# Optimization experiments

Hardware: AMD Instinct MI355X
Metric: run time of the kernel (lower is better)

## Reference

```python
import jax, jax.numpy as jnp
import numpy as np

EPS = 1e-5
G = 8    # groups
K = 3    # kernel_size


def bn(x, gamma, beta, mean, var):
    # inference-mode BatchNorm2d; x: (b,C,H,W), params: (C,)
    inv = gamma / jnp.sqrt(var + EPS)
    return x * inv[None, :, None, None] + (beta - mean * inv)[None, :, None, None]


def gconv1x1(x, w):
    # grouped 1x1 conv; x: (b, g*ci, H, W), w: (g, co, ci) -> (b, g*co, H, W)
    b, C, H, W = x.shape
    g, co, ci = w.shape
    xg = x.reshape(b, g, ci, H, W)
    y = jnp.einsum('bgihw,goi->bgohw', xg, w)
    return y.reshape(b, g * co, H, W)


def unfold3(x):
    # torch.nn.Unfold(k=3, stride=1, dilation=1, padding=1), reshaped to (b, C, 9, H, W)
    b, C, H, W = x.shape
    xp = jnp.pad(x, ((0, 0), (0, 0), (1, 1), (1, 1)))
    patches = [xp[:, :, i:i + H, j:j + W] for i in range(K) for j in range(K)]
    return jnp.stack(patches, axis=2)


def setup_inputs() -> dict:
    key = jax.random.key(0)
    ks = jax.random.split(key, 16)
    f = jax.random.normal
    u = jax.random.uniform
    return {
        'x':  f(ks[0], (2, 256, 128, 128), jnp.float32),
        'w1': f(ks[1], (8, 8, 32), jnp.float32) * 0.1,
        'b1': f(ks[2], (64,), jnp.float32) * 0.1,
        'g1': u(ks[3], (64,), jnp.float32, 0.5, 1.5),
        'be1': f(ks[4], (64,), jnp.float32) * 0.1,
        'm1': f(ks[5], (64,), jnp.float32) * 0.1,
        'v1': u(ks[6], (64,), jnp.float32, 0.5, 1.5),
        'w2': f(ks[7], (8, 10, 8), jnp.float32) * 0.1,
        'b2': f(ks[8], (80,), jnp.float32) * 0.1,
        'g2': u(ks[9], (80,), jnp.float32, 0.5, 1.5),
        'be2': f(ks[10], (80,), jnp.float32) * 0.1,
        'm2': f(ks[11], (80,), jnp.float32) * 0.1,
        'v2': u(ks[12], (80,), jnp.float32, 0.5, 1.5),
        'wv': f(ks[13], (8, 32, 32), jnp.float32) * 0.1,
    }


def reference(x, w1, b1, g1, be1, m1, v1, w2, b2, g2, be2, m2, v2, wv):
    b, C, H, W = x.shape
    # mask_conv: grouped 1x1 conv -> BN -> tanh -> grouped 1x1 conv -> BN
    t = jnp.tanh(bn(gconv1x1(x, w1) + b1[None, :, None, None], g1, be1, m1, v1))
    mn = bn(gconv1x1(t, w2) + b2[None, :, None, None], g2, be2, m2, v2)  # (b, G*(1+K*K), H, W)
    neighbor = mn[:, :G]          # (b, G, H, W)
    mask = mn[:, G:]              # (b, G*K*K, H, W)
    nb = unfold3(neighbor)        # (b, G, 9, H, W)
    logits = mask.reshape(b, G, K * K, H, W) + nb
    attn = jax.nn.softmax(logits, axis=2)               # (b, G, 9, H, W)
    # value path: grouped 1x1 conv (no bias) then unfold
    v = gconv1x1(x, wv)                                  # (b, C, H, W)
    vu = unfold3(v).reshape(b, G, C // G, K * K, H, W)   # (b, G, C/G, 9, H, W)
    out = jnp.einsum('bgkhw,bgckhw->bgchw', attn, vu)    # weighted sum over window
    return out.reshape(b, C, H, W)
```

## Files before the change

kernel.cpp:

```cpp
#include <hip/hip_runtime.h>

#define HW  16384
#define WD  128

#define TS   16
#define HS   18
#define HP   (HS * HS)
#define PRS  20
#define PLS  360

__device__ __forceinline__ unsigned short f2bf(float f) {
    unsigned int u = __builtin_bit_cast(unsigned int, f);
    u += 0x7FFFu + ((u >> 16) & 1u);
    return (unsigned short)(u >> 16);
}
__device__ __forceinline__ float bf2f(unsigned int s) {
    return __builtin_bit_cast(float, (s & 0xFFFFu) << 16);
}
__device__ __forceinline__ float ftanh(float v) {
    const float e = __expf(2.0f * v);
    return 1.0f - __fdividef(2.0f, e + 1.0f);
}

__global__ __launch_bounds__(256) void la_t(
    const float* __restrict__ x,
    const float* __restrict__ w1, const float* __restrict__ b1,
    const float* __restrict__ g1, const float* __restrict__ be1,
    const float* __restrict__ m1, const float* __restrict__ v1,
    ushort4* __restrict__ t4)
{
    const int pix = blockIdx.x * blockDim.x + threadIdx.x;
    const int b   = blockIdx.y;
    const int z   = blockIdx.z;
    const int p   = z >> 1;
    const int h   = z & 1;

    const float* xp = x + (size_t)(b * 256 + p * 32) * HW + pix;
    float xv[32];
#pragma unroll
    for (int c = 0; c < 32; ++c) xv[c] = xp[(size_t)c * HW];

    const float* w1g = w1 + p * 256 + h * 4 * 32;
    float tv[4];
#pragma unroll
    for (int o = 0; o < 4; ++o) {
        float a = 0.f;
#pragma unroll
        for (int ci = 0; ci < 32; ++ci) a = fmaf(xv[ci], w1g[o * 32 + ci], a);
        const int ch = p * 8 + h * 4 + o;
        const float inv = g1[ch] * rsqrtf(v1[ch] + 1e-5f);
        const float add = be1[ch] + (b1[ch] - m1[ch]) * inv;
        tv[o] = ftanh(fmaf(a, inv, add));
    }

    t4[((size_t)((b * 8 + p) * 2 + h)) * HW + pix] =
        make_ushort4(f2bf(tv[0]), f2bf(tv[1]), f2bf(tv[2]), f2bf(tv[3]));
}

__global__ __launch_bounds__(256, 4) void la_fused(
    const float* __restrict__ x,
    const float* __restrict__ w2, const float* __restrict__ b2,
    const float* __restrict__ g2, const float* __restrict__ be2,
    const float* __restrict__ m2, const float* __restrict__ v2,
    const float* __restrict__ wv,
    const ushort4* __restrict__ t4,
    float* __restrict__ out)
{
    __shared__ ushort4 xt[8 * PLS];
    __shared__ float   nbs[PLS];

    const int tid  = threadIdx.x;
    const int bg   = blockIdx.x;
    const int tile = blockIdx.y;
    const int b    = bg >> 3, g = bg & 7;
    const int ty0  = (tile >> 3) * TS;
    const int tx0  = (tile & 7) * TS;

    const float*   xg  = x  + (size_t)(b * 256 + g * 32) * HW;
    const ushort4* t0  = t4 + (size_t)(b * 16) * HW;

    const float inv2n = g2[g] * rsqrtf(v2[g] + 1e-5f);
    const float add2n = be2[g] + (b2[g] - m2[g]) * inv2n;

    for (int hp = tid; hp < HP; hp += 256) {
        const int hy = hp / HS, hx = hp - hy * HS;
        const int iy = ty0 + hy - 1, ix = tx0 + hx - 1;
        const int slot = hy * PRS + hx;
        if (((unsigned)iy < 128u) && ((unsigned)ix < 128u)) {
            const int po = iy * WD + ix;
            float xv[32];
#pragma unroll
            for (int c = 0; c < 32; ++c) xv[c] = xg[(size_t)c * HW + po];
            const ushort4 ta = t0[po];
            const ushort4 tb = t0[(size_t)HW + po];
            float an = 0.f;
            an = fmaf(bf2f(ta.x), w2[g * 8 + 0], an);
            an = fmaf(bf2f(ta.y), w2[g * 8 + 1], an);
            an = fmaf(bf2f(ta.z), w2[g * 8 + 2], an);
            an = fmaf(bf2f(ta.w), w2[g * 8 + 3], an);
            an = fmaf(bf2f(tb.x), w2[g * 8 + 4], an);
            an = fmaf(bf2f(tb.y), w2[g * 8 + 5], an);
            an = fmaf(bf2f(tb.z), w2[g * 8 + 6], an);
            an = fmaf(bf2f(tb.w), w2[g * 8 + 7], an);
            nbs[slot] = fmaf(an, inv2n, add2n);
#pragma unroll
            for (int c4 = 0; c4 < 8; ++c4)
                xt[c4 * PLS + slot] = make_ushort4(
                    f2bf(xv[c4 * 4 + 0]), f2bf(xv[c4 * 4 + 1]),
                    f2bf(xv[c4 * 4 + 2]), f2bf(xv[c4 * 4 + 3]));
        } else {
            const ushort4 z = make_ushort4(0, 0, 0, 0);
#pragma unroll
            for (int c4 = 0; c4 < 8; ++c4) xt[c4 * PLS + slot] = z;
            nbs[slot] = 0.f;
        }
    }
    __syncthreads();

    const int cy  = tid >> 4, cx = tid & 15;
    const int iy  = ty0 + cy, ix = tx0 + cx;
    const int pix = iy * WD + ix;

    const int mc0    = 8 + 9 * g;
    const int pa     = mc0 / 10;
    const int pb     = (mc0 + 8) / 10;
    const int ksplit = 10 - (mc0 - pa * 10);

    float tA[8], tB[8];
    {
        const ushort4 lo = t4[((size_t)((b * 8 + pa) * 2 + 0)) * HW + pix];
        const ushort4 hi = t4[((size_t)((b * 8 + pa) * 2 + 1)) * HW + pix];
        tA[0] = bf2f(lo.x); tA[1] = bf2f(lo.y);
        tA[2] = bf2f(lo.z); tA[3] = bf2f(lo.w);
        tA[4] = bf2f(hi.x); tA[5] = bf2f(hi.y);
        tA[6] = bf2f(hi.z); tA[7] = bf2f(hi.w);
    }
    if (pb != pa) {
        const ushort4 lo = t4[((size_t)((b * 8 + pb) * 2 + 0)) * HW + pix];
        const ushort4 hi = t4[((size_t)((b * 8 + pb) * 2 + 1)) * HW + pix];
        tB[0] = bf2f(lo.x); tB[1] = bf2f(lo.y);
        tB[2] = bf2f(lo.z); tB[3] = bf2f(lo.w);
        tB[4] = bf2f(hi.x); tB[5] = bf2f(hi.y);
        tB[6] = bf2f(hi.z); tB[7] = bf2f(hi.w);
    } else {
#pragma unroll
        for (int o = 0; o < 8; ++o) tB[o] = tA[o];
    }

    float lg[9];
    float mx = -1e30f;
#pragma unroll
    for (int k = 0; k < 9; ++k) {
        const int mc = mc0 + k;
        const int p  = (k < ksplit) ? pa : pb;
        const int o  = mc - p * 10;
        const float* w2p = w2 + p * 80 + o * 8;
        float a = 0.f;
#pragma unroll
        for (int i = 0; i < 8; ++i) {
            const float ti = (k < ksplit) ? tA[i] : tB[i];
            a = fmaf(ti, w2p[i], a);
        }
        const float inv = g2[mc] * rsqrtf(v2[mc] + 1e-5f);
        const float add = be2[mc] + (b2[mc] - m2[mc]) * inv;
        lg[k] = fmaf(a, inv, add) + nbs[(cy + k / 3) * PRS + (cx + k % 3)];
        mx = fmaxf(mx, lg[k]);
    }
    float ssum = 0.f;
#pragma unroll
    for (int k = 0; k < 9; ++k) { lg[k] = __expf(lg[k] - mx); ssum += lg[k]; }
    const float rs = 1.f / ssum;

    float s[32];
#pragma unroll
    for (int c = 0; c < 32; ++c) s[c] = 0.f;
#pragma unroll
    for (int k = 0; k < 9; ++k) {
        const int slot = (cy + k / 3) * PRS + (cx + k % 3);
        const float e = lg[k];
#pragma unroll
        for (int c4 = 0; c4 < 8; ++c4) {
            const ushort4 xv4 = xt[c4 * PLS + slot];
            s[c4 * 4 + 0] = fmaf(e, bf2f(xv4.x), s[c4 * 4 + 0]);
            s[c4 * 4 + 1] = fmaf(e, bf2f(xv4.y), s[c4 * 4 + 1]);
            s[c4 * 4 + 2] = fmaf(e, bf2f(xv4.z), s[c4 * 4 + 2]);
            s[c4 * 4 + 3] = fmaf(e, bf2f(xv4.w), s[c4 * 4 + 3]);
        }
    }

    const float* wvg = wv + g * 1024;
    float* og = out + (size_t)(b * 256 + g * 32) * HW + pix;
#pragma unroll 4
    for (int o = 0; o < 32; ++o) {
        const float* wp = wvg + o * 32;
        float a = 0.f;
#pragma unroll
        for (int ci = 0; ci < 32; ++ci) a = fmaf(s[ci], wp[ci], a);
        __builtin_nontemporal_store(a * rs, og + (size_t)o * HW);
    }
}

extern "C" void kernel_launch(void* const* d_in, const int* in_sizes, int n_in,
                              void* d_out, int out_size, void* d_ws, size_t ws_size,
                              hipStream_t stream)
{
    const float* x   = (const float*)d_in[0];
    const float* w1  = (const float*)d_in[1];
    const float* b1  = (const float*)d_in[2];
    const float* g1  = (const float*)d_in[3];
    const float* be1 = (const float*)d_in[4];
    const float* m1  = (const float*)d_in[5];
    const float* v1  = (const float*)d_in[6];
    const float* w2  = (const float*)d_in[7];
    const float* b2  = (const float*)d_in[8];
    const float* g2  = (const float*)d_in[9];
    const float* be2 = (const float*)d_in[10];
    const float* m2  = (const float*)d_in[11];
    const float* v2  = (const float*)d_in[12];
    const float* wv  = (const float*)d_in[13];

    float* out = (float*)d_out;
    ushort4* t4 = (ushort4*)d_ws;

    dim3 blk(256);
    dim3 gt(HW / 256, 2, 16);
    dim3 grd(16, 64);

    hipLaunchKernelGGL(la_t, gt, blk, 0, stream,
                       x, w1, b1, g1, be1, m1, v1, t4);
    hipLaunchKernelGGL(la_fused, grd, blk, 0, stream,
                       x, w2, b2, g2, be2, m2, v2, wv, t4, out);
}
```

Measured before the change: 126.8 us.

## Precompute bf16 copy of x in first kernel and split output channels across blocks

The first kernel now also writes a bf16 copy of x to workspace, so the fused kernel reads compact bf16 halo data instead of fp32 x. The fused kernel's grid is doubled, with each block computing only 16 of the 32 output channels of the value projection. This cuts the fused kernel's read traffic and per-block register work, and raises parallelism. The cost is an extra bf16 write and read of x, duplicated halo/softmax work across the two half-blocks, and dropping the occupancy hint from the launch bounds.

```diff
diff --git a/kernel.cpp b/kernel.cpp
--- a/kernel.cpp
+++ b/kernel.cpp
@@ -27,7 +27,7 @@
     const float* __restrict__ w1, const float* __restrict__ b1,
     const float* __restrict__ g1, const float* __restrict__ be1,
     const float* __restrict__ m1, const float* __restrict__ v1,
-    ushort4* __restrict__ t4)
+    ushort4* __restrict__ t4, ushort4* __restrict__ xbf)
 {
     const int pix = blockIdx.x * blockDim.x + threadIdx.x;
     const int b   = blockIdx.y;
@@ -40,6 +40,14 @@
 #pragma unroll
     for (int c = 0; c < 32; ++c) xv[c] = xp[(size_t)c * HW];
 
+#pragma unroll
+    for (int j = 0; j < 4; ++j) {
+        const int c4 = h * 4 + j;
+        xbf[((size_t)((b * 8 + p) * 8 + c4)) * HW + pix] = make_ushort4(
+            f2bf(xv[c4 * 4 + 0]), f2bf(xv[c4 * 4 + 1]),
+            f2bf(xv[c4 * 4 + 2]), f2bf(xv[c4 * 4 + 3]));
+    }
+
     const float* w1g = w1 + p * 256 + h * 4 * 32;
     float tv[4];
 #pragma unroll
@@ -57,27 +65,27 @@
         make_ushort4(f2bf(tv[0]), f2bf(tv[1]), f2bf(tv[2]), f2bf(tv[3]));
 }
 
-__global__ __launch_bounds__(256, 4) void la_fused(
-    const float* __restrict__ x,
+__global__ __launch_bounds__(256) void la_fused(
     const float* __restrict__ w2, const float* __restrict__ b2,
     const float* __restrict__ g2, const float* __restrict__ be2,
     const float* __restrict__ m2, const float* __restrict__ v2,
     const float* __restrict__ wv,
-    const ushort4* __restrict__ t4,
+    const ushort4* __restrict__ t4, const ushort4* __restrict__ xbf,
     float* __restrict__ out)
 {
     __shared__ ushort4 xt[8 * PLS];
     __shared__ float   nbs[PLS];
 
     const int tid  = threadIdx.x;
-    const int bg   = blockIdx.x;
+    const int y    = blockIdx.x;
     const int tile = blockIdx.y;
+    const int bg   = y >> 1, h = y & 1;
     const int b    = bg >> 3, g = bg & 7;
     const int ty0  = (tile >> 3) * TS;
     const int tx0  = (tile & 7) * TS;
 
-    const float*   xg  = x  + (size_t)(b * 256 + g * 32) * HW;
-    const ushort4* t0  = t4 + (size_t)(b * 16) * HW;
+    const ushort4* xg = xbf + (size_t)((b * 8 + g) * 8) * HW;
+    const ushort4* t0 = t4  + (size_t)(b * 16) * HW;
 
     const float inv2n = g2[g] * rsqrtf(v2[g] + 1e-5f);
     const float add2n = be2[g] + (b2[g] - m2[g]) * inv2n;
@@ -88,9 +96,6 @@
         const int slot = hy * PRS + hx;
         if (((unsigned)iy < 128u) && ((unsigned)ix < 128u)) {
             const int po = iy * WD + ix;
-            float xv[32];
-#pragma unroll
-            for (int c = 0; c < 32; ++c) xv[c] = xg[(size_t)c * HW + po];
             const ushort4 ta = t0[po];
             const ushort4 tb = t0[(size_t)HW + po];
             float an = 0.f;
@@ -105,9 +110,7 @@
             nbs[slot] = fmaf(an, inv2n, add2n);
 #pragma unroll
             for (int c4 = 0; c4 < 8; ++c4)
-                xt[c4 * PLS + slot] = make_ushort4(
-                    f2bf(xv[c4 * 4 + 0]), f2bf(xv[c4 * 4 + 1]),
-                    f2bf(xv[c4 * 4 + 2]), f2bf(xv[c4 * 4 + 3]));
+                xt[c4 * PLS + slot] = xg[(size_t)c4 * HW + po];
         } else {
             const ushort4 z = make_ushort4(0, 0, 0, 0);
 #pragma unroll
@@ -188,10 +191,10 @@
         }
     }
 
-    const float* wvg = wv + g * 1024;
-    float* og = out + (size_t)(b * 256 + g * 32) * HW + pix;
+    const float* wvg = wv + g * 1024 + h * 16 * 32;
+    float* og = out + (size_t)(b * 256 + g * 32 + h * 16) * HW + pix;
 #pragma unroll 4
-    for (int o = 0; o < 32; ++o) {
+    for (int o = 0; o < 16; ++o) {
         const float* wp = wvg + o * 32;
         float a = 0.f;
 #pragma unroll
@@ -220,14 +223,15 @@
     const float* wv  = (const float*)d_in[13];
 
     float* out = (float*)d_out;
-    ushort4* t4 = (ushort4*)d_ws;
+    ushort4* t4  = (ushort4*)d_ws;
+    ushort4* xbf = t4 + (size_t)32 * HW;
 
     dim3 blk(256);
     dim3 gt(HW / 256, 2, 16);
-    dim3 grd(16, 64);
+    dim3 gfd(32, 64);
 
     hipLaunchKernelGGL(la_t, gt, blk, 0, stream,
-                       x, w1, b1, g1, be1, m1, v1, t4);
-    hipLaunchKernelGGL(la_fused, grd, blk, 0, stream,
-                       x, w2, b2, g2, be2, m2, v2, wv, t4, out);
-}
+                       x, w1, b1, g1, be1, m1, v1, t4, xbf);
+    hipLaunchKernelGGL(la_fused, gfd, blk, 0, stream,
+                       w2, b2, g2, be2, m2, v2, wv, t4, xbf, out);
+}
```

After: 134.5 us. 6.1% more time.
